# Kernel tuning notes

Hardware: AMD Instinct MI355X
Metric: run time of the kernel (lower is better)

Reference implementation:

```python
import jax, jax.numpy as jnp
import numpy as np

S, R, NUM_LORA = 16384, 64, 8
NQ, NKV = 4096, 1024
OUT_DIM = NQ + 2 * NKV
BS, MAX_LEN = 32, 512


def setup_inputs() -> dict:
    key = jax.random.key(0)
    k1, k2, k3, k4, k5, k6 = jax.random.split(key, 6)
    x = jax.random.normal(k1, (S, 3 * R), dtype=jnp.float32)
    qkv_lora_b = jax.random.normal(k2, (NUM_LORA, OUT_DIM, R), dtype=jnp.float32) * 0.02
    seg_indptr = (jnp.arange(BS + 1, dtype=jnp.int32) * MAX_LEN)
    seg_lens = jax.random.randint(k3, (BS,), 256, MAX_LEN + 1, dtype=jnp.int32)
    weight_indices = jax.random.randint(k4, (BS,), 0, NUM_LORA, dtype=jnp.int32)
    # ranks in [0, R]; rank 0 means the segment is a no-op
    lora_ranks = jax.random.randint(k5, (NUM_LORA,), 0, R + 1, dtype=jnp.int32)
    scalings = jax.random.uniform(k6, (NUM_LORA,), minval=0.25, maxval=2.0, dtype=jnp.float32)
    output_offset = jnp.array([0, NQ, NQ + NKV, OUT_DIM], dtype=jnp.int32)
    return {
        "x": x,
        "qkv_lora_b": qkv_lora_b,
        "use_cuda_graph": False,
        "bs": BS,
        "num_segments": BS,
        "seg_indptr": seg_indptr,
        "weight_indices": weight_indices,
        "lora_ranks": lora_ranks,
        "scalings": scalings,
        "max_len": MAX_LEN,
        "seg_lens": seg_lens,
        "permutation": jnp.arange(BS, dtype=jnp.int32),
        "output_offset": output_offset,
        "max_qkv_out_dim": NQ,
    }


def _qkv_lora_b(x, qkv_lora_b, bs, seg_indptr, weight_indices, lora_ranks,
                scalings, max_len, seg_lens, offs):
    s = x.shape[0]
    out_dim, r = qkv_lora_b.shape[1], qkv_lora_b.shape[2]
    L = max_len
    w_idx = weight_indices[:bs]                      # (bs,)
    W = qkv_lora_b[w_idx]                            # (bs, out_dim, r)
    keff = jnp.minimum(r, lora_ranks[w_idx])         # effective rank per segment
    scale = scalings[w_idx]                          # (bs,)
    # gather padded per-segment token blocks
    pos = seg_indptr[:bs, None] + jnp.arange(L, dtype=seg_indptr.dtype)[None, :]   # (bs, L)
    valid = jnp.arange(L)[None, :] < seg_lens[:bs, None]                            # (bs, L)
    Xp = jnp.where(valid[..., None], x[jnp.clip(pos, 0, s - 1)], 0.0)               # (bs, L, 3r)
    # x columns for qkv slice q are [q*keff, q*keff + keff) (packed with stride keff)
    kidx = jnp.arange(r, dtype=jnp.int32)
    cols = jnp.arange(3, dtype=jnp.int32)[None, :, None] * keff[:, None, None] + kidx[None, None, :]  # (bs,3,r)
    kmask = kidx[None, None, :] < keff[:, None, None]
    cols = jnp.where(kmask, cols, 0)
    Xg = jnp.take_along_axis(Xp[:, :, None, :],
                             jnp.broadcast_to(cols[:, None], (bs, L, 3, r)), axis=3)  # (bs, L, 3, r)
    Xg = Xg * kmask[:, None].astype(Xg.dtype)
    # 3 packed GEMMs against the statically-partitioned B weight (Q / K / V rows)
    parts = [jnp.einsum('blk,bnk->bln', Xg[:, :, q], W[:, offs[q]:offs[q + 1], :])
             for q in range(3)]
    seg_out = jnp.concatenate(parts, axis=-1) * scale[:, None, None]    # (bs, L, out_dim)
    # masked scatter-add back into the flat output buffer
    pos_safe = jnp.where(valid, pos, s)   # out-of-range index -> dropped
    out = jnp.zeros((s, out_dim), dtype=x.dtype)
    out = out.at[pos_safe.reshape(-1)].add(seg_out.reshape(-1, out_dim), mode='drop')
    return out


def reference(x, qkv_lora_b, use_cuda_graph, bs, num_segments, seg_indptr,
              weight_indices, lora_ranks, scalings, max_len, seg_lens,
              permutation, output_offset, max_qkv_out_dim):
    offs = np.asarray(jax.device_get(output_offset))  # static [0, Nq, Nq+Nkv, out_dim]
    return _qkv_lora_b(x, qkv_lora_b, int(bs), seg_indptr, weight_indices,
                       lora_ranks, scalings, int(max_len), seg_lens, offs)
```

## Files before the change

kernel.cpp:

```cpp
#include <hip/hip_runtime.h>
#include <stddef.h>

#define SROWS   16384
#define ODIM    6144
#define RMAX    64
#define SEGLEN  512
#define TM      64
#define TN      128

typedef float f4_t __attribute__((ext_vector_type(4)));

__global__ __launch_bounds__(256, 3) void lora_qkv_b_kernel(
    const float* __restrict__ x,
    const float* __restrict__ w_all,
    const int*   __restrict__ weight_indices,
    const int*   __restrict__ lora_ranks,
    const float* __restrict__ scalings,
    const int*   __restrict__ seg_lens,
    float*       __restrict__ out)
{
    __shared__ float xs[TM][RMAX];
    __shared__ float wlds[RMAX][TN + 4];

    const int rb = blockIdx.x;
    const int cb = blockIdx.y;
    const int i0 = rb * TM;
    const int n0 = cb * TN;

    const int seg  = i0 >> 9;
    const int l0   = i0 & (SEGLEN - 1);
    const int w    = weight_indices[seg];
    int keff       = lora_ranks[w];
    if (keff > RMAX) keff = RMAX;
    const float scale = scalings[w];
    const int slen    = seg_lens[seg];

    const int tid    = threadIdx.x;
    const int rbase  = (tid >> 5) * 8;
    const int nlocal = (tid & 31) * 4;

    if (keff == 0 || l0 >= slen) {
        const f4_t z = (f4_t)0.f;
        #pragma unroll
        for (int r = 0; r < 8; ++r) {
            const size_t row = (size_t)(i0 + rbase + r);
            __builtin_nontemporal_store(z, (f4_t*)(out + row * ODIM + n0 + nlocal));
        }
        return;
    }

    const int q    = (n0 < 4096) ? 0 : ((n0 < 5120) ? 1 : 2);
    const int qoff = q * keff;
    const float* Wb = w_all + ((size_t)w * ODIM + n0) * RMAX;

    for (int idx = tid * 4; idx < TN * RMAX; idx += 256 * 4) {
        const int n  = idx >> 6;
        const int k0 = idx & 63;
        float4 v = make_float4(0.f, 0.f, 0.f, 0.f);
        if (k0 < keff) {
            v = *(const float4*)(Wb + (size_t)n * RMAX + k0);
            if (k0 + 1 >= keff) v.y = 0.f;
            if (k0 + 2 >= keff) v.z = 0.f;
            if (k0 + 3 >= keff) v.w = 0.f;
        }
        wlds[k0 + 0][n] = v.x;
        wlds[k0 + 1][n] = v.y;
        wlds[k0 + 2][n] = v.z;
        wlds[k0 + 3][n] = v.w;
    }

    for (int idx = tid; idx < TM * RMAX; idx += 256) {
        const int r = idx >> 6;
        const int k = idx & 63;
        float v = 0.f;
        if (k < keff && (l0 + r) < slen) {
            v = x[(size_t)(i0 + r) * 192 + qoff + k];
        }
        xs[r][k] = v;
    }

    float acc[8][4];
    #pragma unroll
    for (int r = 0; r < 8; ++r)
        #pragma unroll
        for (int c = 0; c < 4; ++c) acc[r][c] = 0.f;

    __syncthreads();

    const int keff4 = (keff + 3) & ~3;
    for (int k = 0; k < keff4; k += 4) {
        const float4 w0 = *(const float4*)(&wlds[k + 0][nlocal]);
        const float4 w1 = *(const float4*)(&wlds[k + 1][nlocal]);
        const float4 w2 = *(const float4*)(&wlds[k + 2][nlocal]);
        const float4 w3 = *(const float4*)(&wlds[k + 3][nlocal]);
        #pragma unroll
        for (int r = 0; r < 8; ++r) {
            const float4 xv = *(const float4*)(&xs[rbase + r][k]);
            acc[r][0] += xv.x * w0.x; acc[r][1] += xv.x * w0.y;
            acc[r][2] += xv.x * w0.z; acc[r][3] += xv.x * w0.w;
            acc[r][0] += xv.y * w1.x; acc[r][1] += xv.y * w1.y;
            acc[r][2] += xv.y * w1.z; acc[r][3] += xv.y * w1.w;
            acc[r][0] += xv.z * w2.x; acc[r][1] += xv.z * w2.y;
            acc[r][2] += xv.z * w2.z; acc[r][3] += xv.z * w2.w;
            acc[r][0] += xv.w * w3.x; acc[r][1] += xv.w * w3.y;
            acc[r][2] += xv.w * w3.z; acc[r][3] += xv.w * w3.w;
        }
    }

    #pragma unroll
    for (int r = 0; r < 8; ++r) {
        const size_t row = (size_t)(i0 + rbase + r);
        f4_t o;
        o.x = acc[r][0] * scale;
        o.y = acc[r][1] * scale;
        o.z = acc[r][2] * scale;
        o.w = acc[r][3] * scale;
        __builtin_nontemporal_store(o, (f4_t*)(out + row * ODIM + n0 + nlocal));
    }
}

extern "C" void kernel_launch(void* const* d_in, const int* in_sizes, int n_in,
                              void* d_out, int out_size, void* d_ws, size_t ws_size,
                              hipStream_t stream) {
    const float* x    = (const float*)d_in[0];
    const float* wb   = (const float*)d_in[1];
    const int*   widx = (const int*)d_in[6];
    const int*   rks  = (const int*)d_in[7];
    const float* scl  = (const float*)d_in[8];
    const int*   sln  = (const int*)d_in[10];
    float* out = (float*)d_out;

    dim3 grid(SROWS / TM, ODIM / TN);
    lora_qkv_b_kernel<<<grid, 256, 0, stream>>>(x, wb, widx, rks, scl, sln, out);
}
```

Baseline: 552.2 us.

## Process four row tiles per block to reuse staged weights and prefetch x

```diff
diff --git a/kernel.cpp b/kernel.cpp
--- a/kernel.cpp
+++ b/kernel.cpp
@@ -7,6 +7,7 @@
 #define SEGLEN  512
 #define TM      64
 #define TN      128
+#define XDIM    192
 
 typedef float f4_t __attribute__((ext_vector_type(4)));
 
@@ -22,13 +23,13 @@
     __shared__ float xs[TM][RMAX];
     __shared__ float wlds[RMAX][TN + 4];
 
-    const int rb = blockIdx.x;
-    const int cb = blockIdx.y;
-    const int i0 = rb * TM;
-    const int n0 = cb * TN;
+    const int seg   = blockIdx.x;
+    const int cb    = blockIdx.y;
+    const int half  = blockIdx.z;
+    const int n0    = cb * TN;
+    const int segbase = seg * SEGLEN;
+    const int lbase = half * (SEGLEN / 2);
 
-    const int seg  = i0 >> 9;
-    const int l0   = i0 & (SEGLEN - 1);
     const int w    = weight_indices[seg];
     int keff       = lora_ranks[w];
     if (keff > RMAX) keff = RMAX;
@@ -39,12 +40,14 @@
     const int rbase  = (tid >> 5) * 8;
     const int nlocal = (tid & 31) * 4;
 
-    if (keff == 0 || l0 >= slen) {
+    if (keff == 0 || lbase >= slen) {
         const f4_t z = (f4_t)0.f;
-        #pragma unroll
-        for (int r = 0; r < 8; ++r) {
-            const size_t row = (size_t)(i0 + rbase + r);
-            __builtin_nontemporal_store(z, (f4_t*)(out + row * ODIM + n0 + nlocal));
+        for (int c = 0; c < 4; ++c) {
+            const int i0 = segbase + lbase + c * TM;
+            #pragma unroll
+            for (int r = 0; r < 8; ++r)
+                __builtin_nontemporal_store(
+                    z, (f4_t*)(out + (size_t)(i0 + rbase + r) * ODIM + n0 + nlocal));
         }
         return;
     }
@@ -69,53 +72,84 @@
         wlds[k0 + 3][n] = v.w;
     }
 
-    for (int idx = tid; idx < TM * RMAX; idx += 256) {
-        const int r = idx >> 6;
-        const int k = idx & 63;
-        float v = 0.f;
-        if (k < keff && (l0 + r) < slen) {
-            v = x[(size_t)(i0 + r) * 192 + qoff + k];
-        }
-        xs[r][k] = v;
+    const int kk = tid & 63;
+    const int r0 = tid >> 6;
+    const int keff4 = (keff + 3) & ~3;
+
+    float pref[16];
+    {
+        const float* p = x + ((size_t)(segbase + lbase) + r0) * XDIM + qoff + kk;
+        #pragma unroll
+        for (int m = 0; m < 16; ++m) pref[m] = p[(size_t)m * 4 * XDIM];
     }
 
-    float acc[8][4];
-    #pragma unroll
-    for (int r = 0; r < 8; ++r)
+    for (int c = 0; c < 4; ++c) {
+        const int l0 = lbase + c * TM;
+        const int i0 = segbase + l0;
+
+        if (l0 >= slen) {
+            const f4_t z = (f4_t)0.f;
+            #pragma unroll
+            for (int r = 0; r < 8; ++r)
+                __builtin_nontemporal_store(
+                    z, (f4_t*)(out + (size_t)(i0 + rbase + r) * ODIM + n0 + nlocal));
+            continue;
+        }
+
+        if (l0 + TM <= slen) {
+            #pragma unroll
+            for (int m = 0; m < 16; ++m) xs[m * 4 + r0][kk] = pref[m];
+        } else {
+            #pragma unroll
+            for (int m = 0; m < 16; ++m)
+                xs[m * 4 + r0][kk] = (l0 + m * 4 + r0 < slen) ? pref[m] : 0.f;
+        }
+
+        __syncthreads();
+
+        if (c < 3 && l0 + TM < slen) {
+            const float* p = x + ((size_t)(i0 + TM) + r0) * XDIM + qoff + kk;
+            #pragma unroll
+            for (int m = 0; m < 16; ++m) pref[m] = p[(size_t)m * 4 * XDIM];
+        }
+
+        float acc[8][4];
         #pragma unroll
-        for (int c = 0; c < 4; ++c) acc[r][c] = 0.f;
+        for (int r = 0; r < 8; ++r)
+            #pragma unroll
+            for (int cc = 0; cc < 4; ++cc) acc[r][cc] = 0.f;
 
-    __syncthreads();
+        for (int k = 0; k < keff4; k += 4) {
+            const float4 w0 = *(const float4*)(&wlds[k + 0][nlocal]);
+            const float4 w1 = *(const float4*)(&wlds[k + 1][nlocal]);
+            const float4 w2 = *(const float4*)(&wlds[k + 2][nlocal]);
+            const float4 w3 = *(const float4*)(&wlds[k + 3][nlocal]);
+            #pragma unroll
+            for (int r = 0; r < 8; ++r) {
+                const float4 xv = *(const float4*)(&xs[rbase + r][k]);
+                acc[r][0] += xv.x * w0.x; acc[r][1] += xv.x * w0.y;
+                acc[r][2] += xv.x * w0.z; acc[r][3] += xv.x * w0.w;
+                acc[r][0] += xv.y * w1.x; acc[r][1] += xv.y * w1.y;
+                acc[r][2] += xv.y * w1.z; acc[r][3] += xv.y * w1.w;
+                acc[r][0] += xv.z * w2.x; acc[r][1] += xv.z * w2.y;
+                acc[r][2] += xv.z * w2.z; acc[r][3] += xv.z * w2.w;
+                acc[r][0] += xv.w * w3.x; acc[r][1] += xv.w * w3.y;
+                acc[r][2] += xv.w * w3.z; acc[r][3] += xv.w * w3.w;
+            }
+        }
 
-    const int keff4 = (keff + 3) & ~3;
-    for (int k = 0; k < keff4; k += 4) {
-        const float4 w0 = *(const float4*)(&wlds[k + 0][nlocal]);
-        const float4 w1 = *(const float4*)(&wlds[k + 1][nlocal]);
-        const float4 w2 = *(const float4*)(&wlds[k + 2][nlocal]);
-        const float4 w3 = *(const float4*)(&wlds[k + 3][nlocal]);
+        __syncthreads();
+
         #pragma unroll
         for (int r = 0; r < 8; ++r) {
-            const float4 xv = *(const float4*)(&xs[rbase + r][k]);
-            acc[r][0] += xv.x * w0.x; acc[r][1] += xv.x * w0.y;
-            acc[r][2] += xv.x * w0.z; acc[r][3] += xv.x * w0.w;
-            acc[r][0] += xv.y * w1.x; acc[r][1] += xv.y * w1.y;
-            acc[r][2] += xv.y * w1.z; acc[r][3] += xv.y * w1.w;
-            acc[r][0] += xv.z * w2.x; acc[r][1] += xv.z * w2.y;
-            acc[r][2] += xv.z * w2.z; acc[r][3] += xv.z * w2.w;
-            acc[r][0] += xv.w * w3.x; acc[r][1] += xv.w * w3.y;
-            acc[r][2] += xv.w * w3.z; acc[r][3] += xv.w * w3.w;
+            const size_t row = (size_t)(i0 + rbase + r);
+            f4_t o;
+            o.x = acc[r][0] * scale;
+            o.y = acc[r][1] * scale;
+            o.z = acc[r][2] * scale;
+            o.w = acc[r][3] * scale;
+            __builtin_nontemporal_store(o, (f4_t*)(out + row * ODIM + n0 + nlocal));
         }
-    }
-
-    #pragma unroll
-    for (int r = 0; r < 8; ++r) {
-        const size_t row = (size_t)(i0 + rbase + r);
-        f4_t o;
-        o.x = acc[r][0] * scale;
-        o.y = acc[r][1] * scale;
-        o.z = acc[r][2] * scale;
-        o.w = acc[r][3] * scale;
-        __builtin_nontemporal_store(o, (f4_t*)(out + row * ODIM + n0 + nlocal));
     }
 }
 
@@ -130,6 +164,6 @@
     const int*   sln  = (const int*)d_in[10];
     float* out = (float*)d_out;
 
-    dim3 grid(SROWS / TM, ODIM / TN);
+    dim3 grid(32, ODIM / TN, 2);
     lora_qkv_b_kernel<<<grid, 256, 0, stream>>>(x, wb, widx, rks, scl, sln, out);
 }
```

Result: faster. 483.7 us (-12.4%).
